# Performance work log

Measured on AMD Instinct MI355X. Metric: run time of the kernel, lower is better.

## Reference

```python
import jax, jax.numpy as jnp
import numpy as np

EPS = 1e-8


def _autocorr2d(x):
    # x: [B, H, W] single-channel batch
    B, H, W = x.shape
    xc = x - x.mean(axis=(-2, -1), keepdims=True)
    # torch.std defaults to unbiased (ddof=1)
    xn = xc / (xc.std(axis=(-2, -1), ddof=1, keepdims=True) + EPS)
    ph, pw = H // 4, W // 4
    # grouped cross-correlation: input [1,B,H,W], kernel [B,1,H,W], groups=B
    # (lax conv, like torch conv2d, does NOT flip the kernel)
    corr = jax.lax.conv_general_dilated(
        xn[None],            # [1, B, H, W]
        xn[:, None],         # [B, 1, H, W]
        window_strides=(1, 1),
        padding=((ph, ph), (pw, pw)),
        feature_group_count=B,
        dimension_numbers=('NCHW', 'OIHW', 'NCHW'),
    )  # [1, B, 2*(H//4)+1, 2*(W//4)+1]
    norm = jnp.sqrt(jnp.sum(xn ** 2, axis=(-2, -1))).reshape(B, 1, 1, 1)
    # Faithful to the original: [1,B,oh,ow] / [B,1,1,1] broadcasts to [B,B,oh,ow]
    # (the torch .squeeze(0) is a no-op on the resulting shape)
    return corr / (norm + EPS)


def _channel_mean_corr(x):
    # x: [B, C, H, W] -> mean over channels of per-channel autocorr -> [B, B, oh, ow]
    return jax.vmap(_autocorr2d, in_axes=1)(x).mean(axis=0)


def setup_inputs() -> dict:
    key = jax.random.key(0)
    k1, k2 = jax.random.split(key)
    B, C, H, W = 8, 3, 192, 192
    pred = jax.random.normal(k1, (B, C, H, W), dtype=jnp.float32)
    target = jax.random.normal(k2, (B, C, H, W), dtype=jnp.float32)
    return {"pred": pred, "target": target}


def reference(pred, target):
    pred_corr = _channel_mean_corr(pred)
    target_corr = _channel_mean_corr(target)
    pred_corr = pred_corr / (pred_corr.max() + EPS)
    target_corr = target_corr / (target_corr.max() + EPS)
    return jnp.mean(jnp.abs(pred_corr - target_corr))
```

## Files before the change

### kernel.cpp

```cpp
#include <hip/hip_runtime.h>
#include <math.h>

#define EPSF 1e-8f
#define HW 36864
#define SHALF 4753
#define NIDX (8*SHALF)

#define OFF_INV   0
#define OFF_NORM  48
#define OFF_MAX   144
#define OFF_ACC   146
#define OFF_CNT   147
#define OFF_PART  160
#define OFF_CTR   256
#define OFF_S     1024
#define OFF_PREP  229168

#define CY 12
#define AROWS 75
#define APITCH 400
#define CPB 720
#define RB 5824
#define ABYTES 30000
#define BBYTES (4*RB)
#define LDSB (ABYTES + BBYTES)

#define MAXB 64
#define LOSSB 64

typedef short short8 __attribute__((ext_vector_type(8)));
typedef float f32x4 __attribute__((ext_vector_type(4)));

__device__ __forceinline__ unsigned int pk2(float a, float b) {
  union { float f; unsigned int u; } x, y;
  x.f = a; y.f = b;
  unsigned int ra = x.u + 0x7fffu + ((x.u >> 16) & 1u);
  unsigned int rb = y.u + 0x7fffu + ((y.u >> 16) & 1u);
  return (ra >> 16) | (rb & 0xffff0000u);
}

__global__ __launch_bounds__(256) void stats_prep(const float* __restrict__ pred,
                                                  const float* __restrict__ target,
                                                  float* __restrict__ ws) {
  int blk = blockIdx.x, tid = threadIdx.x;
  int img = blk >> 2, qtr = blk & 3;
  int t = img / 24, local = img % 24;
  const float* src = (t ? target : pred) + (size_t)local * HW + qtr * 9216;

  float* S = ws + OFF_S;
  for (int i = blk * 256 + tid; i < 48 * SHALF; i += 192 * 256) S[i] = 0.f;

  const float4* s4 = (const float4*)src;
  float s = 0.f, sq = 0.f;
  for (int i = tid; i < 2304; i += 256) {
    float4 v = s4[i];
    s  += (v.x + v.y) + (v.z + v.w);
    sq += (v.x*v.x + v.y*v.y) + (v.z*v.z + v.w*v.w);
  }
#pragma unroll
  for (int o = 32; o > 0; o >>= 1) { s += __shfl_down(s, o); sq += __shfl_down(sq, o); }
  __shared__ float rs[4], rq[4], bcast[1];
  int lane = tid & 63, wv = tid >> 6;
  if (!lane) { rs[wv] = s; rq[wv] = sq; }
  __syncthreads();
  if (!tid) {
    s  = (rs[0] + rs[1]) + (rs[2] + rs[3]);
    sq = (rq[0] + rq[1]) + (rq[2] + rq[3]);
    atomicAdd(&ws[OFF_PART + 2*img],     s);
    atomicAdd(&ws[OFF_PART + 2*img + 1], sq);
    __threadfence();
    atomicAdd((int*)ws + OFF_CTR + img, 1);
    while (atomicAdd((int*)ws + OFF_CTR + img, 0) < 4) { }
    float S1 = atomicAdd(&ws[OFF_PART + 2*img],     0.f);
    float Q  = atomicAdd(&ws[OFF_PART + 2*img + 1], 0.f);
    float mean = S1 / (float)HW;
    float M2 = fmaxf(Q - S1 * S1 / (float)HW, 0.f);
    float inv = 1.f / (sqrtf(M2 / (float)(HW - 1)) + EPSF);
    bcast[0] = mean;
    if (qtr == 0) {
      ws[OFF_INV  + img] = inv;
      ws[OFF_NORM + img] = sqrtf(M2) * inv;
    }
  }
  __syncthreads();
  float mean = bcast[0];

  unsigned short* prep = (unsigned short*)(ws + OFF_PREP) + (size_t)img * HW + qtr * 9216;
  for (int i = tid; i < 2304; i += 256) {
    float4 v = s4[i];
    uint2 d; d.x = pk2(v.x - mean, v.y - mean); d.y = pk2(v.z - mean, v.w - mean);
    *(uint2*)(prep + i * 4) = d;
  }
}

__global__ __launch_bounds__(256, 3) void autocorr_mfma(float* __restrict__ ws) {
  int blk = blockIdx.x;
  int img = blk >> 4, chunk = blk & 15;
  int Y = chunk * CY;
  const unsigned short* prep = (const unsigned short*)(ws + OFF_PREP) + (size_t)img * HW;
  float inv = ws[OFF_INV + img];
  float scale = inv * inv;

  __shared__ __align__(16) char lds[LDSB];
  char* Al = lds;
  char* Bl = lds + ABYTES;

  int tid = threadIdx.x;
  int w = tid >> 6, lane = tid & 63, c = lane & 15, h = lane >> 4;

  int RV = 192 - Y;
  for (int m = tid; m < 1800; m += 256) {
    int r = m / 24, k = m - r * 24;
    short8 v = (short8)(short)0;
    if (r < RV) v = *(const short8*)(prep + (Y + r) * 192 + k * 8);
    *(short8*)(Al + r * APITCH + k * 16) = v;
  }

  int p_l = (8 - (c & 7)) & 7;
  int q_l = (c == 0) ? 0 : ((c <= 8) ? 1 : 2);
  int pad_l = (p_l == 0) ? 16 : ((p_l & 1) ? 80 : 32);
  int LB0 = p_l * CPB + pad_l + 16 * (h - q_l) + 128;

  f32x4 acc[4][7];
#pragma unroll
  for (int mt = 0; mt < 4; mt++)
#pragma unroll
    for (int nt = 0; nt < 7; nt++) acc[mt][nt] = (f32x4)0.f;

  for (int j = 0; j < 3; ++j) {
    __syncthreads();
    if (tid < 180) {
      int rr = tid / 45, k = tid - rr * 45;
      const unsigned short* srow = prep + (Y + 4 * j + rr) * 192;
      int e0 = 8 * k - 112;
      unsigned short q[15];
#pragma unroll
      for (int i2 = 0; i2 < 15; i2++) {
        int x = e0 + i2;
        q[i2] = ((unsigned)x < 192u) ? srow[x] : (unsigned short)0;
      }
      unsigned int D[8], Sh[7];
#pragma unroll
      for (int a2 = 0; a2 < 7; a2++) D[a2] = (unsigned)q[2*a2] | ((unsigned)q[2*a2+1] << 16);
      D[7] = (unsigned)q[14];
#pragma unroll
      for (int b2 = 0; b2 < 7; b2++) Sh[b2] = (D[b2] >> 16) | (D[b2+1] << 16);
      char* base = Bl + rr * RB + k * 16;
#pragma unroll
      for (int p = 0; p < 8; p++) {
        int pb = (p == 0) ? 16 : ((p & 1) ? 80 : 32);
        int4 v;
        if ((p & 1) == 0) { v.x = (int)D[p/2]; v.y = (int)D[p/2+1]; v.z = (int)D[p/2+2]; v.w = (int)D[p/2+3]; }
        else { v.x = (int)Sh[(p-1)/2]; v.y = (int)Sh[(p-1)/2+1]; v.z = (int)Sh[(p-1)/2+2]; v.w = (int)Sh[(p-1)/2+3]; }
        *(int4*)(base + p * CPB + pb) = v;
      }
    }
    __syncthreads();

    const char* pB = Bl + w * RB + LB0;
    const char* pA = Al + ((4 * j + w) + c) * APITCH + 16 * h;
    short8 Wf[17];
#pragma unroll
    for (int wi = 0; wi < 7; wi++) Wf[wi] = *(const short8*)(pB + 32 * wi);
#pragma unroll
    for (int t = 0; t < 6; t++) {
      if (t) {
        Wf[2*t+5] = *(const short8*)(pB + 32 * (2*t+5));
        Wf[2*t+6] = *(const short8*)(pB + 32 * (2*t+6));
      }
#pragma unroll
      for (int mt = 0; mt < 4; mt++) {
        short8 Af = *(const short8*)(pA + mt * (16 * APITCH) + 64 * t);
#pragma unroll
        for (int nt = 0; nt < 7; nt++)
          acc[mt][nt] = __builtin_amdgcn_mfma_f32_16x16x32_bf16(Af, Wf[2*t+6-nt], acc[mt][nt], 0, 0, 0);
      }
    }
  }

  __syncthreads();
  if (w >= 2) {
    char* rg = lds + (w - 2) * 15360 + lane * 240;
#pragma unroll
    for (int mt = 0; mt < 2; mt++)
#pragma unroll
      for (int nt = 0; nt < 7; nt++) *(f32x4*)(rg + (mt*7+nt)*16) = acc[mt][nt];
  }
  __syncthreads();
  if (w < 2) {
    const char* rg = lds + w * 15360 + lane * 240;
#pragma unroll
    for (int mt = 0; mt < 2; mt++)
#pragma unroll
      for (int nt = 0; nt < 7; nt++) {
        f32x4 o = *(const f32x4*)(rg + (mt*7+nt)*16);
        acc[mt][nt][0] += o[0]; acc[mt][nt][1] += o[1]; acc[mt][nt][2] += o[2]; acc[mt][nt][3] += o[3];
      }
  }
  __syncthreads();
  if (w >= 2) {
    char* rg = lds + (w - 2) * 15360 + lane * 240;
#pragma unroll
    for (int mt = 2; mt < 4; mt++)
#pragma unroll
      for (int nt = 0; nt < 7; nt++) *(f32x4*)(rg + ((mt-2)*7+nt)*16) = acc[mt][nt];
  }
  __syncthreads();
  if (w < 2) {
    const char* rg = lds + w * 15360 + lane * 240;
#pragma unroll
    for (int mt = 2; mt < 4; mt++)
#pragma unroll
      for (int nt = 0; nt < 7; nt++) {
        f32x4 o = *(const f32x4*)(rg + ((mt-2)*7+nt)*16);
        acc[mt][nt][0] += o[0]; acc[mt][nt][1] += o[1]; acc[mt][nt][2] += o[2]; acc[mt][nt][3] += o[3];
      }
  }
  __syncthreads();
  if (w == 1) {
    char* rg = lds + lane * 240;
#pragma unroll
    for (int mt = 0; mt < 2; mt++)
#pragma unroll
      for (int nt = 0; nt < 7; nt++) *(f32x4*)(rg + (mt*7+nt)*16) = acc[mt][nt];
  }
  if (w == 0) {
    char* rg = lds + 15360 + lane * 240;
#pragma unroll
    for (int mt = 2; mt < 4; mt++)
#pragma unroll
      for (int nt = 0; nt < 7; nt++) *(f32x4*)(rg + ((mt-2)*7+nt)*16) = acc[mt][nt];
  }
  __syncthreads();
  float* S2 = ws + OFF_S + (size_t)img * SHALF;
  if (w == 0) {
    const char* rg = lds + lane * 240;
#pragma unroll
    for (int mt = 0; mt < 2; mt++)
#pragma unroll
      for (int nt = 0; nt < 7; nt++) {
        f32x4 o = *(const f32x4*)(rg + (mt*7+nt)*16);
        int s = 16 * nt + c;
#pragma unroll
        for (int r = 0; r < 4; r++) {
          int sy = 16 * mt + 4 * h + r;
          if (sy <= 48 && s <= 96)
            atomicAdd(&S2[sy * 97 + s], (acc[mt][nt][r] + o[r]) * scale);
        }
      }
  } else if (w == 1) {
    const char* rg = lds + 15360 + lane * 240;
#pragma unroll
    for (int mt = 2; mt < 4; mt++)
#pragma unroll
      for (int nt = 0; nt < 7; nt++) {
        f32x4 o = *(const f32x4*)(rg + ((mt-2)*7+nt)*16);
        int s = 16 * nt + c;
#pragma unroll
        for (int r = 0; r < 4; r++) {
          int sy = 16 * mt + 4 * h + r;
          if (sy <= 48 && s <= 96)
            atomicAdd(&S2[sy * 97 + s], (acc[mt][nt][r] + o[r]) * scale);
        }
      }
  }
}

__global__ __launch_bounds__(256) void max_kernel(float* __restrict__ ws) {
  __shared__ float wsh[48];
  int tid = threadIdx.x;
  if (tid < 48) wsh[tid] = (1.f / 3.f) / (ws[OFF_NORM + tid] + EPSF);
  __syncthreads();
  float mp = 0.f, mt2 = 0.f;
  const float* S = ws + OFF_S;
  for (int idx = blockIdx.x * 256 + tid; idx < NIDX; idx += MAXB * 256) {
    int j = idx / SHALF, off = idx - j * SHALF;
    const float* Pp = S + (size_t)(3 * j) * SHALF + off;
    const float* Tt = S + (size_t)(24 + 3 * j) * SHALF + off;
    float p0 = Pp[0], p1 = Pp[SHALF], p2 = Pp[2 * SHALF];
    float q0 = Tt[0], q1 = Tt[SHALF], q2 = Tt[2 * SHALF];
#pragma unroll
    for (int i = 0; i < 8; i++) {
      float pv = p0 * wsh[i*3] + p1 * wsh[i*3+1] + p2 * wsh[i*3+2];
      float tv = q0 * wsh[24+i*3] + q1 * wsh[24+i*3+1] + q2 * wsh[24+i*3+2];
      mp = fmaxf(mp, pv); mt2 = fmaxf(mt2, tv);
    }
  }
#pragma unroll
  for (int o = 32; o > 0; o >>= 1) { mp = fmaxf(mp, __shfl_down(mp, o)); mt2 = fmaxf(mt2, __shfl_down(mt2, o)); }
  __shared__ float rp[4], rt[4];
  int lane = tid & 63, wv = tid >> 6;
  if (!lane) { rp[wv] = mp; rt[wv] = mt2; }
  __syncthreads();
  if (!tid) {
    mp  = fmaxf(fmaxf(rp[0], rp[1]), fmaxf(rp[2], rp[3]));
    mt2 = fmaxf(fmaxf(rt[0], rt[1]), fmaxf(rt[2], rt[3]));
    atomicMax((int*)ws + OFF_MAX,     __float_as_int(mp));
    atomicMax((int*)ws + OFF_MAX + 1, __float_as_int(mt2));
  }
}

__global__ __launch_bounds__(256) void loss_final(float* __restrict__ ws,
                                                  float* __restrict__ out) {
  __shared__ float wsh[48];
  int tid = threadIdx.x;
  if (tid < 48) wsh[tid] = (1.f / 3.f) / (ws[OFF_NORM + tid] + EPSF);
  __syncthreads();
  float imp = 1.f / (__int_as_float(((const int*)ws)[OFF_MAX])     + EPSF);
  float imt = 1.f / (__int_as_float(((const int*)ws)[OFF_MAX + 1]) + EPSF);
  float acc = 0.f;
  const float* S = ws + OFF_S;
  for (int idx = blockIdx.x * 256 + tid; idx < NIDX; idx += LOSSB * 256) {
    int j = idx / SHALF, off = idx - j * SHALF;
    float wgt = (off < 97) ? 1.f : 2.f;
    const float* Pp = S + (size_t)(3 * j) * SHALF + off;
    const float* Tt = S + (size_t)(24 + 3 * j) * SHALF + off;
    float p0 = Pp[0], p1 = Pp[SHALF], p2 = Pp[2 * SHALF];
    float q0 = Tt[0], q1 = Tt[SHALF], q2 = Tt[2 * SHALF];
    float a8 = 0.f;
#pragma unroll
    for (int i = 0; i < 8; i++) {
      float pv = (p0 * wsh[i*3] + p1 * wsh[i*3+1] + p2 * wsh[i*3+2]) * imp;
      float tv = (q0 * wsh[24+i*3] + q1 * wsh[24+i*3+1] + q2 * wsh[24+i*3+2]) * imt;
      a8 += fabsf(pv - tv);
    }
    acc += wgt * a8;
  }
#pragma unroll
  for (int o = 32; o > 0; o >>= 1) acc += __shfl_down(acc, o);
  __shared__ float r[4];
  int lane = tid & 63, wv = tid >> 6;
  if (!lane) r[wv] = acc;
  __syncthreads();
  if (!tid) {
    float bs = (r[0] + r[1]) + (r[2] + r[3]);
    atomicAdd(&ws[OFF_ACC], bs);
    __threadfence();
    int old = atomicAdd((int*)ws + OFF_CNT, 1);
    if (old == LOSSB - 1) {
      float total = atomicAdd(&ws[OFF_ACC], 0.f);
      out[0] = total * (1.0f / 602176.0f);
    }
  }
}

extern "C" void kernel_launch(void* const* d_in, const int* in_sizes, int n_in,
                              void* d_out, int out_size, void* d_ws, size_t ws_size,
                              hipStream_t stream) {
  const float* pred   = (const float*)d_in[0];
  const float* target = (const float*)d_in[1];
  float* ws  = (float*)d_ws;
  float* out = (float*)d_out;

  hipMemsetAsync((char*)d_ws + 144 * sizeof(float), 0, (304 - 144) * sizeof(float), stream);
  hipLaunchKernelGGL(stats_prep,    dim3(192),     dim3(256), 0, stream, pred, target, ws);
  hipLaunchKernelGGL(autocorr_mfma, dim3(48 * 16), dim3(256), 0, stream, ws);
  hipLaunchKernelGGL(max_kernel,    dim3(MAXB),    dim3(256), 0, stream, ws);
  hipLaunchKernelGGL(loss_final,    dim3(LOSSB),   dim3(256), 0, stream, ws, out);
}
```

Measured before the change: 71.64 us.

## Replace atomic accumulation with per-chunk partials and fuse max and loss kernels

```diff
diff --git a/kernel.cpp b/kernel.cpp
--- a/kernel.cpp
+++ b/kernel.cpp
@@ -4,29 +4,27 @@
 #define EPSF 1e-8f
 #define HW 36864
 #define SHALF 4753
-#define NIDX (8*SHALF)
-
-#define OFF_INV   0
-#define OFF_NORM  48
-#define OFF_MAX   144
-#define OFF_ACC   146
-#define OFF_CNT   147
-#define OFF_PART  160
-#define OFF_CTR   256
-#define OFF_S     1024
-#define OFF_PREP  229168
+
+#define OFF_INV    0
+#define OFF_NORM   48
+#define OFF_MAX    144
+#define OFF_ACC    146
+#define OFF_CNT2   147
+#define OFF_CNT3   148
+#define OFF_PART   160
+#define OFF_CTR    256
+#define OFF_PARTS  1024
+#define OFF_PREP   3651328
 
 #define CY 12
-#define AROWS 75
+#define AR 61
 #define APITCH 400
 #define CPB 720
 #define RB 5824
-#define ABYTES 30000
+#define ABYTES (AR*APITCH)
 #define BBYTES (4*RB)
 #define LDSB (ABYTES + BBYTES)
-
-#define MAXB 64
-#define LOSSB 64
+#define ESTR 272
 
 typedef short short8 __attribute__((ext_vector_type(8)));
 typedef float f32x4 __attribute__((ext_vector_type(4)));
@@ -46,9 +44,6 @@
   int img = blk >> 2, qtr = blk & 3;
   int t = img / 24, local = img % 24;
   const float* src = (t ? target : pred) + (size_t)local * HW + qtr * 9216;
-
-  float* S = ws + OFF_S;
-  for (int i = blk * 256 + tid; i < 48 * SHALF; i += 192 * 256) S[i] = 0.f;
 
   const float4* s4 = (const float4*)src;
   float s = 0.f, sq = 0.f;
@@ -84,7 +79,6 @@
   }
   __syncthreads();
   float mean = bcast[0];
-
   unsigned short* prep = (unsigned short*)(ws + OFF_PREP) + (size_t)img * HW + qtr * 9216;
   for (int i = tid; i < 2304; i += 256) {
     float4 v = s4[i];
@@ -93,7 +87,7 @@
   }
 }
 
-__global__ __launch_bounds__(256, 3) void autocorr_mfma(float* __restrict__ ws) {
+__global__ __launch_bounds__(256, 2) void autocorr_mfma(float* __restrict__ ws) {
   int blk = blockIdx.x;
   int img = blk >> 4, chunk = blk & 15;
   int Y = chunk * CY;
@@ -109,43 +103,35 @@
   int w = tid >> 6, lane = tid & 63, c = lane & 15, h = lane >> 4;
 
   int RV = 192 - Y;
-  for (int m = tid; m < 1800; m += 256) {
+  for (int m = tid; m < AR * 24; m += 256) {
     int r = m / 24, k = m - r * 24;
     short8 v = (short8)(short)0;
     if (r < RV) v = *(const short8*)(prep + (Y + r) * 192 + k * 8);
     *(short8*)(Al + r * APITCH + k * 16) = v;
   }
 
-  int p_l = (8 - (c & 7)) & 7;
-  int q_l = (c == 0) ? 0 : ((c <= 8) ? 1 : 2);
-  int pad_l = (p_l == 0) ? 16 : ((p_l & 1) ? 80 : 32);
-  int LB0 = p_l * CPB + pad_l + 16 * (h - q_l) + 128;
-
-  f32x4 acc[4][7];
-#pragma unroll
-  for (int mt = 0; mt < 4; mt++)
-#pragma unroll
-    for (int nt = 0; nt < 7; nt++) acc[mt][nt] = (f32x4)0.f;
-
-  for (int j = 0; j < 3; ++j) {
-    __syncthreads();
+  int srr = tid / 45, sk = tid - srr * 45;
+  unsigned short q[15];
+  auto stage_load = [&](int jd) {
     if (tid < 180) {
-      int rr = tid / 45, k = tid - rr * 45;
-      const unsigned short* srow = prep + (Y + 4 * j + rr) * 192;
-      int e0 = 8 * k - 112;
-      unsigned short q[15];
+      const unsigned short* srow = prep + (Y + 4 * jd + srr) * 192;
+      int e0 = 8 * sk - 112;
 #pragma unroll
       for (int i2 = 0; i2 < 15; i2++) {
         int x = e0 + i2;
         q[i2] = ((unsigned)x < 192u) ? srow[x] : (unsigned short)0;
       }
+    }
+  };
+  auto stage_write = [&]() {
+    if (tid < 180) {
       unsigned int D[8], Sh[7];
 #pragma unroll
       for (int a2 = 0; a2 < 7; a2++) D[a2] = (unsigned)q[2*a2] | ((unsigned)q[2*a2+1] << 16);
       D[7] = (unsigned)q[14];
 #pragma unroll
       for (int b2 = 0; b2 < 7; b2++) Sh[b2] = (D[b2] >> 16) | (D[b2+1] << 16);
-      char* base = Bl + rr * RB + k * 16;
+      char* base = Bl + srr * RB + sk * 16;
 #pragma unroll
       for (int p = 0; p < 8; p++) {
         int pb = (p == 0) ? 16 : ((p & 1) ? 80 : 32);
@@ -155,32 +141,54 @@
         *(int4*)(base + p * CPB + pb) = v;
       }
     }
+  };
+
+  int p_l = (8 - (c & 7)) & 7;
+  int q_l = (c == 0) ? 0 : ((c <= 8) ? 1 : 2);
+  int pad_l = (p_l == 0) ? 16 : ((p_l & 1) ? 80 : 32);
+  int LB0 = p_l * CPB + pad_l + 16 * (h - q_l) + 128;
+
+  f32x4 acc[4][7];
+#pragma unroll
+  for (int mt = 0; mt < 4; mt++)
+#pragma unroll
+    for (int nt = 0; nt < 7; nt++) acc[mt][nt] = (f32x4)0.f;
+
+  stage_load(0);
+  for (int j = 0; j < 3; ++j) {
     __syncthreads();
+    stage_write();
+    __syncthreads();
+    if (j < 2) stage_load(j + 1);
 
     const char* pB = Bl + w * RB + LB0;
-    const char* pA = Al + ((4 * j + w) + c) * APITCH + 16 * h;
-    short8 Wf[17];
+    int rb[4];
+#pragma unroll
+    for (int mt = 0; mt < 4; mt++) {
+      int ra = 4 * j + w + 16 * mt + c;
+      rb[mt] = (ra > 60 ? 60 : ra) * APITCH + 16 * h;
+    }
+    short8 Wf[8];
 #pragma unroll
     for (int wi = 0; wi < 7; wi++) Wf[wi] = *(const short8*)(pB + 32 * wi);
 #pragma unroll
     for (int t = 0; t < 6; t++) {
-      if (t) {
-        Wf[2*t+5] = *(const short8*)(pB + 32 * (2*t+5));
-        Wf[2*t+6] = *(const short8*)(pB + 32 * (2*t+6));
-      }
-#pragma unroll
-      for (int mt = 0; mt < 4; mt++) {
-        short8 Af = *(const short8*)(pA + mt * (16 * APITCH) + 64 * t);
+      if (t < 5) Wf[(2*t+7) & 7] = *(const short8*)(pB + 32 * (2*t+7));
+      short8 Af[4];
+#pragma unroll
+      for (int mt = 0; mt < 4; mt++) Af[mt] = *(const short8*)(Al + rb[mt] + 64 * t);
+#pragma unroll
+      for (int mt = 0; mt < 4; mt++)
 #pragma unroll
         for (int nt = 0; nt < 7; nt++)
-          acc[mt][nt] = __builtin_amdgcn_mfma_f32_16x16x32_bf16(Af, Wf[2*t+6-nt], acc[mt][nt], 0, 0, 0);
-      }
+          acc[mt][nt] = __builtin_amdgcn_mfma_f32_16x16x32_bf16(Af[mt], Wf[(2*t+6-nt) & 7], acc[mt][nt], 0, 0, 0);
+      if (t < 5) Wf[(2*t+8) & 7] = *(const short8*)(pB + 32 * (2*t+8));
     }
   }
 
   __syncthreads();
   if (w >= 2) {
-    char* rg = lds + (w - 2) * 15360 + lane * 240;
+    char* rg = lds + (w - 2) * 17408 + lane * ESTR;
 #pragma unroll
     for (int mt = 0; mt < 2; mt++)
 #pragma unroll
@@ -188,7 +196,7 @@
   }
   __syncthreads();
   if (w < 2) {
-    const char* rg = lds + w * 15360 + lane * 240;
+    const char* rg = lds + w * 17408 + lane * ESTR;
 #pragma unroll
     for (int mt = 0; mt < 2; mt++)
 #pragma unroll
@@ -199,7 +207,7 @@
   }
   __syncthreads();
   if (w >= 2) {
-    char* rg = lds + (w - 2) * 15360 + lane * 240;
+    char* rg = lds + (w - 2) * 17408 + lane * ESTR;
 #pragma unroll
     for (int mt = 2; mt < 4; mt++)
 #pragma unroll
@@ -207,7 +215,7 @@
   }
   __syncthreads();
   if (w < 2) {
-    const char* rg = lds + w * 15360 + lane * 240;
+    const char* rg = lds + w * 17408 + lane * ESTR;
 #pragma unroll
     for (int mt = 2; mt < 4; mt++)
 #pragma unroll
@@ -218,73 +226,86 @@
   }
   __syncthreads();
   if (w == 1) {
-    char* rg = lds + lane * 240;
+    char* rg = lds + lane * ESTR;
 #pragma unroll
     for (int mt = 0; mt < 2; mt++)
 #pragma unroll
       for (int nt = 0; nt < 7; nt++) *(f32x4*)(rg + (mt*7+nt)*16) = acc[mt][nt];
   }
   if (w == 0) {
-    char* rg = lds + 15360 + lane * 240;
+    char* rg = lds + 17408 + lane * ESTR;
 #pragma unroll
     for (int mt = 2; mt < 4; mt++)
 #pragma unroll
       for (int nt = 0; nt < 7; nt++) *(f32x4*)(rg + ((mt-2)*7+nt)*16) = acc[mt][nt];
   }
   __syncthreads();
-  float* S2 = ws + OFF_S + (size_t)img * SHALF;
+  float* part = ws + OFF_PARTS + (size_t)(img * 16 + chunk) * SHALF;
   if (w == 0) {
-    const char* rg = lds + lane * 240;
+    const char* rg = lds + lane * ESTR;
 #pragma unroll
     for (int mt = 0; mt < 2; mt++)
 #pragma unroll
       for (int nt = 0; nt < 7; nt++) {
         f32x4 o = *(const f32x4*)(rg + (mt*7+nt)*16);
         int s = 16 * nt + c;
-#pragma unroll
-        for (int r = 0; r < 4; r++) {
-          int sy = 16 * mt + 4 * h + r;
-          if (sy <= 48 && s <= 96)
-            atomicAdd(&S2[sy * 97 + s], (acc[mt][nt][r] + o[r]) * scale);
-        }
+        if (s <= 96)
+#pragma unroll
+          for (int r = 0; r < 4; r++) {
+            int sy = 16 * mt + 4 * h + r;
+            part[sy * 97 + s] = (acc[mt][nt][r] + o[r]) * scale;
+          }
       }
   } else if (w == 1) {
-    const char* rg = lds + 15360 + lane * 240;
+    const char* rg = lds + 17408 + lane * ESTR;
 #pragma unroll
     for (int mt = 2; mt < 4; mt++)
 #pragma unroll
       for (int nt = 0; nt < 7; nt++) {
         f32x4 o = *(const f32x4*)(rg + ((mt-2)*7+nt)*16);
         int s = 16 * nt + c;
-#pragma unroll
-        for (int r = 0; r < 4; r++) {
-          int sy = 16 * mt + 4 * h + r;
-          if (sy <= 48 && s <= 96)
-            atomicAdd(&S2[sy * 97 + s], (acc[mt][nt][r] + o[r]) * scale);
-        }
-      }
-  }
-}
-
-__global__ __launch_bounds__(256) void max_kernel(float* __restrict__ ws) {
+        if (s <= 96)
+#pragma unroll
+          for (int r = 0; r < 4; r++) {
+            int sy = 32 + 16 * (mt - 2) + 4 * h + r;
+            if (sy <= 48)
+              part[sy * 97 + s] = (acc[mt][nt][r] + o[r]) * scale;
+          }
+      }
+  }
+}
+
+__global__ __launch_bounds__(256) void post_kernel(float* __restrict__ ws,
+                                                   float* __restrict__ out) {
   __shared__ float wsh[48];
+  __shared__ float shv[2];
   int tid = threadIdx.x;
   if (tid < 48) wsh[tid] = (1.f / 3.f) / (ws[OFF_NORM + tid] + EPSF);
   __syncthreads();
+  int b = blockIdx.x >> 5, seg = blockIdx.x & 31;
+  int off = seg * 149 + tid;
+  bool act = (tid < 149) && (off < SHALF);
+  float p0 = 0.f, p1 = 0.f, p2 = 0.f, q0 = 0.f, q1 = 0.f, q2 = 0.f;
+  if (act) {
+    const float* P = ws + OFF_PARTS;
+    const float* pa = P + (size_t)((3*b + 0) * 16) * SHALF + off;
+    const float* pb = P + (size_t)((3*b + 1) * 16) * SHALF + off;
+    const float* pc = P + (size_t)((3*b + 2) * 16) * SHALF + off;
+    const float* ta = P + (size_t)((24 + 3*b + 0) * 16) * SHALF + off;
+    const float* tb = P + (size_t)((24 + 3*b + 1) * 16) * SHALF + off;
+    const float* tc = P + (size_t)((24 + 3*b + 2) * 16) * SHALF + off;
+#pragma unroll
+    for (int ch = 0; ch < 16; ch++) {
+      p0 += pa[ch * SHALF]; p1 += pb[ch * SHALF]; p2 += pc[ch * SHALF];
+      q0 += ta[ch * SHALF]; q1 += tb[ch * SHALF]; q2 += tc[ch * SHALF];
+    }
+  }
   float mp = 0.f, mt2 = 0.f;
-  const float* S = ws + OFF_S;
-  for (int idx = blockIdx.x * 256 + tid; idx < NIDX; idx += MAXB * 256) {
-    int j = idx / SHALF, off = idx - j * SHALF;
-    const float* Pp = S + (size_t)(3 * j) * SHALF + off;
-    const float* Tt = S + (size_t)(24 + 3 * j) * SHALF + off;
-    float p0 = Pp[0], p1 = Pp[SHALF], p2 = Pp[2 * SHALF];
-    float q0 = Tt[0], q1 = Tt[SHALF], q2 = Tt[2 * SHALF];
-#pragma unroll
-    for (int i = 0; i < 8; i++) {
-      float pv = p0 * wsh[i*3] + p1 * wsh[i*3+1] + p2 * wsh[i*3+2];
-      float tv = q0 * wsh[24+i*3] + q1 * wsh[24+i*3+1] + q2 * wsh[24+i*3+2];
-      mp = fmaxf(mp, pv); mt2 = fmaxf(mt2, tv);
-    }
+#pragma unroll
+  for (int i = 0; i < 8; i++) {
+    float pv = p0 * wsh[i*3] + p1 * wsh[i*3+1] + p2 * wsh[i*3+2];
+    float tv = q0 * wsh[24+i*3] + q1 * wsh[24+i*3+1] + q2 * wsh[24+i*3+2];
+    mp = fmaxf(mp, pv); mt2 = fmaxf(mt2, tv);
   }
 #pragma unroll
   for (int o = 32; o > 0; o >>= 1) { mp = fmaxf(mp, __shfl_down(mp, o)); mt2 = fmaxf(mt2, __shfl_down(mt2, o)); }
@@ -297,26 +318,18 @@
     mt2 = fmaxf(fmaxf(rt[0], rt[1]), fmaxf(rt[2], rt[3]));
     atomicMax((int*)ws + OFF_MAX,     __float_as_int(mp));
     atomicMax((int*)ws + OFF_MAX + 1, __float_as_int(mt2));
-  }
-}
-
-__global__ __launch_bounds__(256) void loss_final(float* __restrict__ ws,
-                                                  float* __restrict__ out) {
-  __shared__ float wsh[48];
-  int tid = threadIdx.x;
-  if (tid < 48) wsh[tid] = (1.f / 3.f) / (ws[OFF_NORM + tid] + EPSF);
-  __syncthreads();
-  float imp = 1.f / (__int_as_float(((const int*)ws)[OFF_MAX])     + EPSF);
-  float imt = 1.f / (__int_as_float(((const int*)ws)[OFF_MAX + 1]) + EPSF);
+    __threadfence();
+    atomicAdd((int*)ws + OFF_CNT2, 1);
+    while (atomicAdd((int*)ws + OFF_CNT2, 0) < 256) { }
+    int mpb = atomicAdd((int*)ws + OFF_MAX, 0);
+    int mtb = atomicAdd((int*)ws + OFF_MAX + 1, 0);
+    shv[0] = 1.f / (__int_as_float(mpb) + EPSF);
+    shv[1] = 1.f / (__int_as_float(mtb) + EPSF);
+  }
+  __syncthreads();
+  float imp = shv[0], imt = shv[1];
   float acc = 0.f;
-  const float* S = ws + OFF_S;
-  for (int idx = blockIdx.x * 256 + tid; idx < NIDX; idx += LOSSB * 256) {
-    int j = idx / SHALF, off = idx - j * SHALF;
-    float wgt = (off < 97) ? 1.f : 2.f;
-    const float* Pp = S + (size_t)(3 * j) * SHALF + off;
-    const float* Tt = S + (size_t)(24 + 3 * j) * SHALF + off;
-    float p0 = Pp[0], p1 = Pp[SHALF], p2 = Pp[2 * SHALF];
-    float q0 = Tt[0], q1 = Tt[SHALF], q2 = Tt[2 * SHALF];
+  if (act) {
     float a8 = 0.f;
 #pragma unroll
     for (int i = 0; i < 8; i++) {
@@ -324,20 +337,19 @@
       float tv = (q0 * wsh[24+i*3] + q1 * wsh[24+i*3+1] + q2 * wsh[24+i*3+2]) * imt;
       a8 += fabsf(pv - tv);
     }
-    acc += wgt * a8;
+    acc = ((off < 97) ? 1.f : 2.f) * a8;
   }
 #pragma unroll
   for (int o = 32; o > 0; o >>= 1) acc += __shfl_down(acc, o);
   __shared__ float r[4];
-  int lane = tid & 63, wv = tid >> 6;
   if (!lane) r[wv] = acc;
   __syncthreads();
   if (!tid) {
     float bs = (r[0] + r[1]) + (r[2] + r[3]);
     atomicAdd(&ws[OFF_ACC], bs);
     __threadfence();
-    int old = atomicAdd((int*)ws + OFF_CNT, 1);
-    if (old == LOSSB - 1) {
+    int old = atomicAdd((int*)ws + OFF_CNT3, 1);
+    if (old == 255) {
       float total = atomicAdd(&ws[OFF_ACC], 0.f);
       out[0] = total * (1.0f / 602176.0f);
     }
@@ -352,9 +364,8 @@
   float* ws  = (float*)d_ws;
   float* out = (float*)d_out;
 
-  hipMemsetAsync((char*)d_ws + 144 * sizeof(float), 0, (304 - 144) * sizeof(float), stream);
+  hipMemsetAsync((char*)d_ws + 144 * sizeof(float), 0, 160 * sizeof(float), stream);
   hipLaunchKernelGGL(stats_prep,    dim3(192),     dim3(256), 0, stream, pred, target, ws);
   hipLaunchKernelGGL(autocorr_mfma, dim3(48 * 16), dim3(256), 0, stream, ws);
-  hipLaunchKernelGGL(max_kernel,    dim3(MAXB),    dim3(256), 0, stream, ws);
-  hipLaunchKernelGGL(loss_final,    dim3(LOSSB),   dim3(256), 0, stream, ws, out);
-}
+  hipLaunchKernelGGL(post_kernel,   dim3(256),     dim3(256), 0, stream, ws, out);
+}
```

Result: slower. 80.65 us (+12.6%).
